# Performance work log

Hardware: AMD Instinct MI355X
Metric: run time of the kernel (lower is better)

## Reference

```python
import jax, jax.numpy as jnp
import numpy as np
import math

HIDDEN = 512
N_PROTO = 1024
BATCH = 16384


def setup_inputs() -> dict:
    key = jax.random.key(0)
    kx, kp = jax.random.split(key)
    X = jax.random.normal(kx, (BATCH, HIDDEN), dtype=jnp.float32)
    # prototypes init: uniform in [-k, k], k = 1/sqrt(hidden)
    k = 1.0 / math.sqrt(HIDDEN)
    u = jax.random.uniform(kp, (N_PROTO, HIDDEN), dtype=jnp.float32)
    prototypes = k + (-2.0 * k) * u
    return {"X": X, "prototypes": prototypes}


def reference(X, prototypes):
    # out[b, p] = -sum_h (X[b,h] - prototypes[p,h])^2
    x_sq = jnp.sum(X * X, axis=1, keepdims=True)            # [B, 1]
    p_sq = jnp.sum(prototypes * prototypes, axis=1)[None, :]  # [1, P]
    cross = jnp.einsum("bh,ph->bp", X, prototypes)          # [B, P]
    return -(x_sq + p_sq - 2.0 * cross)
```

## Files before the change

### kernel.cpp

```cpp
#include <hip/hip_runtime.h>
#include <hip/hip_bf16.h>

#define MDIM 16384
#define NDIM 1024
#define KDIM 512
#define BM 128
#define BN 128
#define BK 64
#define KTILES (KDIM / BK)

typedef __attribute__((ext_vector_type(8))) short bf16x8;
typedef __attribute__((ext_vector_type(4))) float f32x4;

__device__ __forceinline__ short f2bf(float f) {
    union { float f; unsigned u; } v; v.f = f;
    unsigned r = v.u + 0x7fff + ((v.u >> 16) & 1);
    return (short)(r >> 16);
}

__device__ __forceinline__ bf16x8 cvt8(float4 a, float4 b) {
    bf16x8 o;
    o[0] = f2bf(a.x); o[1] = f2bf(a.y); o[2] = f2bf(a.z); o[3] = f2bf(a.w);
    o[4] = f2bf(b.x); o[5] = f2bf(b.y); o[6] = f2bf(b.z); o[7] = f2bf(b.w);
    return o;
}

__device__ __forceinline__ void gload_lds16(const void* g, void* l) {
    __builtin_amdgcn_global_load_lds(
        (const __attribute__((address_space(1))) void*)g,
        (__attribute__((address_space(3))) void*)l, 16, 0, 0);
}

__global__ __launch_bounds__(256) void convert_sumsq(
        const float* __restrict__ X, const float* __restrict__ P,
        short* __restrict__ Xbf, short* __restrict__ Pbf,
        float* __restrict__ xsq, float* __restrict__ psq) {
    int wave = (blockIdx.x * blockDim.x + threadIdx.x) >> 6;
    int lane = threadIdx.x & 63;
    const float* src; short* dstb; float* dsts; int row;
    if (wave < MDIM) { src = X; dstb = Xbf; dsts = xsq; row = wave; }
    else             { src = P; dstb = Pbf; dsts = psq; row = wave - MDIM; }
    const float4* r4 = (const float4*)(src + (size_t)row * KDIM) + lane * 2;
    float4 a = r4[0], b = r4[1];
    *(bf16x8*)(dstb + (size_t)row * KDIM + lane * 8) = cvt8(a, b);
    float s = a.x*a.x + a.y*a.y + a.z*a.z + a.w*a.w
            + b.x*b.x + b.y*b.y + b.z*b.z + b.w*b.w;
    #pragma unroll
    for (int off = 32; off; off >>= 1) s += __shfl_down(s, off, 64);
    if (lane == 0) dsts[row] = s;
}

__global__ __launch_bounds__(512, 4) void dist_gemm_db(
        const short* __restrict__ Xbf, const short* __restrict__ Pbf,
        const float* __restrict__ xsq, const float* __restrict__ psq,
        float* __restrict__ out) {
    __shared__ short As[2][BM * BK];
    __shared__ short Bs[2][BN * BK];

    int tid = threadIdx.x;
    int bid = blockIdx.x;
    int swz = (bid & 7) * 128 + (bid >> 3);
    int bn = swz & 7, bm = swz >> 3;
    int row0 = bm * BM, col0 = bn * BN;

    int lane = tid & 63, wid = tid >> 6;
    int wr = wid >> 2, wc = wid & 3;

    f32x4 acc[4][2] = {};

    const short* Ab = Xbf + (size_t)row0 * KDIM;
    const short* Bb = Pbf + (size_t)col0 * KDIM;

    auto stage = [&](int sel, int kt) {
        #pragma unroll
        for (int s = 0; s < 2; ++s) {
            int c = s * 512 + tid;
            int row = c >> 3;
            int g16 = (c & 7) ^ (row & 7);
            const char* ga = (const char*)(Ab + (size_t)row * KDIM)
                             + (size_t)kt * (BK * 2) + g16 * 16;
            const char* gb = (const char*)(Bb + (size_t)row * KDIM)
                             + (size_t)kt * (BK * 2) + g16 * 16;
            char* la = (char*)&As[sel][0] + s * 8192 + wid * 1024;
            char* lb = (char*)&Bs[sel][0] + s * 8192 + wid * 1024;
            gload_lds16(ga, la);
            gload_lds16(gb, lb);
        }
    };

    auto lds_off = [&](int row, int kb) {
        return (row * (BK * 2) + kb) ^ ((row & 7) << 4);
    };

    auto compute = [&](int sel) {
        const char* aB = (const char*)&As[sel][0];
        const char* bB = (const char*)&Bs[sel][0];
        #pragma unroll
        for (int ks = 0; ks < 2; ++ks) {
            int kb = ks * 64 + ((lane >> 4) * 16);
            bf16x8 af[4], bfr[2];
            #pragma unroll
            for (int m = 0; m < 4; ++m)
                af[m] = *(const bf16x8*)(aB +
                    lds_off(wr * 64 + m * 16 + (lane & 15), kb));
            #pragma unroll
            for (int n = 0; n < 2; ++n)
                bfr[n] = *(const bf16x8*)(bB +
                    lds_off(wc * 32 + n * 16 + (lane & 15), kb));
            #pragma unroll
            for (int m = 0; m < 4; ++m)
                #pragma unroll
                for (int n = 0; n < 2; ++n)
                    acc[m][n] = __builtin_amdgcn_mfma_f32_16x16x32_bf16(
                        af[m], bfr[n], acc[m][n], 0, 0, 0);
        }
    };

    stage(0, 0);
    __syncthreads();
    int cur = 0;
    #pragma unroll
    for (int kt = 0; kt < KTILES - 1; ++kt) {
        stage(cur ^ 1, kt + 1);
        compute(cur);
        __syncthreads();
        cur ^= 1;
    }
    compute(cur);

    int cr = (lane >> 4) * 4;
    int cc = lane & 15;
    float ps[2];
    #pragma unroll
    for (int n = 0; n < 2; ++n) ps[n] = psq[col0 + wc * 32 + n * 16 + cc];
    #pragma unroll
    for (int m = 0; m < 4; ++m) {
        int grb = row0 + wr * 64 + m * 16 + cr;
        #pragma unroll
        for (int r = 0; r < 4; ++r) {
            float xv = xsq[grb + r];
            size_t ob = (size_t)(grb + r) * NDIM;
            #pragma unroll
            for (int n = 0; n < 2; ++n) {
                int gc = col0 + wc * 32 + n * 16 + cc;
                out[ob + gc] = 2.0f * acc[m][n][r] - xv - ps[n];
            }
        }
    }
}

__global__ __launch_bounds__(256) void sumsq_kernel(
        const float* __restrict__ X, const float* __restrict__ P,
        float* __restrict__ xsq, float* __restrict__ psq) {
    int wave = (blockIdx.x * blockDim.x + threadIdx.x) >> 6;
    int lane = threadIdx.x & 63;
    const float* src; float* dst; int row;
    if (wave < MDIM) { src = X; dst = xsq; row = wave; }
    else             { src = P; dst = psq; row = wave - MDIM; }
    const float4* r4 = (const float4*)(src + (size_t)row * KDIM) + lane * 2;
    float4 a = r4[0], b = r4[1];
    float s = a.x*a.x + a.y*a.y + a.z*a.z + a.w*a.w
            + b.x*b.x + b.y*b.y + b.z*b.z + b.w*b.w;
    #pragma unroll
    for (int off = 32; off; off >>= 1) s += __shfl_down(s, off, 64);
    if (lane == 0) dst[row] = s;
}

__global__ __launch_bounds__(256) void dist_gemm(
        const float* __restrict__ X, const float* __restrict__ P,
        const float* __restrict__ xsq, const float* __restrict__ psq,
        float* __restrict__ out) {
    __shared__ short As[128 * BK];
    __shared__ short Bs[128 * BK];
    int tid = threadIdx.x;
    int bid = blockIdx.x;
    int swz = (bid & 7) * 128 + (bid >> 3);
    int bn = swz & 7, bm = swz >> 3;
    int row0 = bm * 128, col0 = bn * 128;
    int lane = tid & 63, wid = tid >> 6;
    int wm = (wid >> 1) * 64, wn = (wid & 1) * 64;
    f32x4 acc[4][4] = {};
    int rbase = tid >> 3;
    int kg = tid & 7;
    const float* Abase = X + (size_t)row0 * KDIM;
    const float* Bbase = P + (size_t)col0 * KDIM;
    for (int kt = 0; kt < KDIM / BK; ++kt) {
        int kofs = kt * BK + kg * 8;
        __syncthreads();
        #pragma unroll
        for (int i = 0; i < 4; ++i) {
            int row = rbase + 32 * i;
            const float4* ga = (const float4*)(Abase + (size_t)row * KDIM + kofs);
            float4 a0 = ga[0], a1 = ga[1];
            const float4* gb = (const float4*)(Bbase + (size_t)row * KDIM + kofs);
            float4 b0 = gb[0], b1 = gb[1];
            int off = (row * (BK * 2) + kg * 16) ^ ((row & 7) << 4);
            *(bf16x8*)((char*)As + off) = cvt8(a0, a1);
            *(bf16x8*)((char*)Bs + off) = cvt8(b0, b1);
        }
        __syncthreads();
        #pragma unroll
        for (int ks = 0; ks < 2; ++ks) {
            bf16x8 af[4], bfr[4];
            int kb = ks * 64 + ((lane >> 4) * 16);
            #pragma unroll
            for (int m = 0; m < 4; ++m) {
                int row = wm + m * 16 + (lane & 15);
                int off = (row * (BK * 2) + kb) ^ ((row & 7) << 4);
                af[m] = *(const bf16x8*)((const char*)As + off);
            }
            #pragma unroll
            for (int n = 0; n < 4; ++n) {
                int row = wn + n * 16 + (lane & 15);
                int off = (row * (BK * 2) + kb) ^ ((row & 7) << 4);
                bfr[n] = *(const bf16x8*)((const char*)Bs + off);
            }
            #pragma unroll
            for (int m = 0; m < 4; ++m)
                #pragma unroll
                for (int n = 0; n < 4; ++n)
                    acc[m][n] = __builtin_amdgcn_mfma_f32_16x16x32_bf16(
                        af[m], bfr[n], acc[m][n], 0, 0, 0);
        }
    }
    int cr = (lane >> 4) * 4;
    int cc = lane & 15;
    #pragma unroll
    for (int n = 0; n < 4; ++n) {
        int gc = col0 + wn + n * 16 + cc;
        float ps = psq[gc];
        #pragma unroll
        for (int m = 0; m < 4; ++m) {
            int grb = row0 + wm + m * 16 + cr;
            #pragma unroll
            for (int r = 0; r < 4; ++r) {
                float v = 2.0f * acc[m][n][r] - xsq[grb + r] - ps;
                out[(size_t)(grb + r) * NDIM + gc] = v;
            }
        }
    }
}

extern "C" void kernel_launch(void* const* d_in, const int* in_sizes, int n_in,
                              void* d_out, int out_size, void* d_ws, size_t ws_size,
                              hipStream_t stream) {
    const float* X = (const float*)d_in[0];
    const float* P = (const float*)d_in[1];
    float* out = (float*)d_out;

    const size_t bf_elems = (size_t)(MDIM + NDIM) * KDIM;
    const size_t need = bf_elems * 2 + (size_t)(MDIM + NDIM) * 4;

    if (ws_size >= need) {
        short* Xbf = (short*)d_ws;
        short* Pbf = Xbf + (size_t)MDIM * KDIM;
        float* xsq = (float*)(Xbf + bf_elems);
        float* psq = xsq + MDIM;
        convert_sumsq<<<(MDIM + NDIM) / 4, 256, 0, stream>>>(X, P, Xbf, Pbf, xsq, psq);
        dist_gemm_db<<<(MDIM / BM) * (NDIM / BN), 512, 0, stream>>>(Xbf, Pbf, xsq, psq, out);
    } else {
        float* xsq = (float*)d_ws;
        float* psq = xsq + MDIM;
        sumsq_kernel<<<(MDIM + NDIM) / 4, 256, 0, stream>>>(X, P, xsq, psq);
        dist_gemm<<<(MDIM / 128) * (NDIM / 128), 256, 0, stream>>>(X, P, xsq, psq, out);
    }
}
```

Measured before the change: 41.10 us.

## Fuse X bf16 conversion and row norms into the distance GEMM

Removes the separate pass that converted all of X to bf16 and computed its row norms. The GEMM kernel now loads fp32 X tiles into registers, converts them and writes them into swizzled LDS, and accumulates row sums of squares on the fly. Only the prototypes still go through a small pre-conversion kernel. The block-to-tile mapping also changes so that the 8 column blocks sharing an X row block run close together. The cost is that every X tile is now read and converted 8 times (once per column block) in fp32, plus extra register pressure and VALU work inside the GEMM.

```diff
diff --git a/kernel.cpp b/kernel.cpp
--- a/kernel.cpp
+++ b/kernel.cpp
@@ -7,9 +7,10 @@
 #define BM 128
 #define BN 128
 #define BK 64
-#define KTILES (KDIM / BK)
+#define KT (KDIM / BK)
 
 typedef __attribute__((ext_vector_type(8))) short bf16x8;
+typedef __attribute__((ext_vector_type(4))) short bf16x4;
 typedef __attribute__((ext_vector_type(4))) float f32x4;
 
 __device__ __forceinline__ short f2bf(float f) {
@@ -31,67 +32,77 @@
         (__attribute__((address_space(3))) void*)l, 16, 0, 0);
 }
 
-__global__ __launch_bounds__(256) void convert_sumsq(
-        const float* __restrict__ X, const float* __restrict__ P,
-        short* __restrict__ Xbf, short* __restrict__ Pbf,
-        float* __restrict__ xsq, float* __restrict__ psq) {
+__global__ __launch_bounds__(256) void convert_p(
+        const float* __restrict__ P, short* __restrict__ Pbf,
+        float* __restrict__ psq) {
     int wave = (blockIdx.x * blockDim.x + threadIdx.x) >> 6;
     int lane = threadIdx.x & 63;
-    const float* src; short* dstb; float* dsts; int row;
-    if (wave < MDIM) { src = X; dstb = Xbf; dsts = xsq; row = wave; }
-    else             { src = P; dstb = Pbf; dsts = psq; row = wave - MDIM; }
-    const float4* r4 = (const float4*)(src + (size_t)row * KDIM) + lane * 2;
+    const float4* r4 = (const float4*)(P + (size_t)wave * KDIM) + lane * 2;
     float4 a = r4[0], b = r4[1];
-    *(bf16x8*)(dstb + (size_t)row * KDIM + lane * 8) = cvt8(a, b);
+    *(bf16x8*)(Pbf + (size_t)wave * KDIM + lane * 8) = cvt8(a, b);
     float s = a.x*a.x + a.y*a.y + a.z*a.z + a.w*a.w
             + b.x*b.x + b.y*b.y + b.z*b.z + b.w*b.w;
     #pragma unroll
     for (int off = 32; off; off >>= 1) s += __shfl_down(s, off, 64);
-    if (lane == 0) dsts[row] = s;
-}
-
-__global__ __launch_bounds__(512, 4) void dist_gemm_db(
-        const short* __restrict__ Xbf, const short* __restrict__ Pbf,
-        const float* __restrict__ xsq, const float* __restrict__ psq,
-        float* __restrict__ out) {
+    if (lane == 0) psq[wave] = s;
+}
+
+__global__ __launch_bounds__(512, 4) void dist_fused2(
+        const float* __restrict__ X, const short* __restrict__ Pbf,
+        const float* __restrict__ psq, float* __restrict__ out) {
     __shared__ short As[2][BM * BK];
     __shared__ short Bs[2][BN * BK];
+    __shared__ float xs_l[BM];
 
     int tid = threadIdx.x;
     int bid = blockIdx.x;
-    int swz = (bid & 7) * 128 + (bid >> 3);
-    int bn = swz & 7, bm = swz >> 3;
-    int row0 = bm * BM, col0 = bn * BN;
+    int x = bid & 7, j = bid >> 3;
+    int colb = j & 7, rowb = x * 16 + (j >> 3);
+    int row0 = rowb * BM, col0 = colb * BN;
 
     int lane = tid & 63, wid = tid >> 6;
     int wr = wid >> 2, wc = wid & 3;
 
     f32x4 acc[4][2] = {};
 
-    const short* Ab = Xbf + (size_t)row0 * KDIM;
+    int arow = tid >> 2, q = tid & 3;
+    const float4* rp4 = (const float4*)(X + (size_t)(row0 + arow) * KDIM);
+    float4 ra[4];
+    float ssq = 0.f;
+
+    auto loadA = [&](int kt) {
+        #pragma unroll
+        for (int i = 0; i < 4; ++i)
+            ra[i] = rp4[kt * 16 + i * 4 + q];
+    };
+    auto commitA = [&](int sel) {
+        #pragma unroll
+        for (int i = 0; i < 4; ++i) {
+            float4 a = ra[i];
+            ssq += a.x * a.x + a.y * a.y + a.z * a.z + a.w * a.w;
+            bf16x4 av;
+            av[0] = f2bf(a.x); av[1] = f2bf(a.y); av[2] = f2bf(a.z); av[3] = f2bf(a.w);
+            int col4 = i * 4 + q;
+            int off = (arow * (BK * 2) + col4 * 8) ^ ((arow & 7) << 4);
+            *(bf16x4*)((char*)&As[sel][0] + off) = av;
+        }
+    };
     const short* Bb = Pbf + (size_t)col0 * KDIM;
-
-    auto stage = [&](int sel, int kt) {
+    auto stageB = [&](int sel, int kt) {
         #pragma unroll
         for (int s = 0; s < 2; ++s) {
             int c = s * 512 + tid;
             int row = c >> 3;
             int g16 = (c & 7) ^ (row & 7);
-            const char* ga = (const char*)(Ab + (size_t)row * KDIM)
-                             + (size_t)kt * (BK * 2) + g16 * 16;
             const char* gb = (const char*)(Bb + (size_t)row * KDIM)
                              + (size_t)kt * (BK * 2) + g16 * 16;
-            char* la = (char*)&As[sel][0] + s * 8192 + wid * 1024;
-            char* lb = (char*)&Bs[sel][0] + s * 8192 + wid * 1024;
-            gload_lds16(ga, la);
-            gload_lds16(gb, lb);
+            gload_lds16(gb, (char*)&Bs[sel][0] + s * 8192 + wid * 1024);
         }
     };
 
     auto lds_off = [&](int row, int kb) {
         return (row * (BK * 2) + kb) ^ ((row & 7) << 4);
     };
-
     auto compute = [&](int sel) {
         const char* aB = (const char*)&As[sel][0];
         const char* bB = (const char*)&Bs[sel][0];
@@ -116,17 +127,26 @@
         }
     };
 
-    stage(0, 0);
+    stageB(0, 0);
+    loadA(0);
+    commitA(0);
     __syncthreads();
-    int cur = 0;
-    #pragma unroll
-    for (int kt = 0; kt < KTILES - 1; ++kt) {
-        stage(cur ^ 1, kt + 1);
+
+    #pragma unroll
+    for (int t = 0; t < KT - 1; ++t) {
+        int cur = t & 1;
+        stageB(cur ^ 1, t + 1);
+        loadA(t + 1);
         compute(cur);
+        commitA(cur ^ 1);
         __syncthreads();
-        cur ^= 1;
-    }
-    compute(cur);
+    }
+    compute((KT - 1) & 1);
+
+    ssq += __shfl_xor(ssq, 1, 64);
+    ssq += __shfl_xor(ssq, 2, 64);
+    if (q == 0) xs_l[arow] = ssq;
+    __syncthreads();
 
     int cr = (lane >> 4) * 4;
     int cc = lane & 15;
@@ -135,16 +155,14 @@
     for (int n = 0; n < 2; ++n) ps[n] = psq[col0 + wc * 32 + n * 16 + cc];
     #pragma unroll
     for (int m = 0; m < 4; ++m) {
-        int grb = row0 + wr * 64 + m * 16 + cr;
         #pragma unroll
         for (int r = 0; r < 4; ++r) {
-            float xv = xsq[grb + r];
-            size_t ob = (size_t)(grb + r) * NDIM;
-            #pragma unroll
-            for (int n = 0; n < 2; ++n) {
-                int gc = col0 + wc * 32 + n * 16 + cc;
-                out[ob + gc] = 2.0f * acc[m][n][r] - xv - ps[n];
-            }
+            int lr = wr * 64 + m * 16 + cr + r;
+            float xv = xs_l[lr];
+            size_t ob = (size_t)(row0 + lr) * NDIM + col0;
+            #pragma unroll
+            for (int n = 0; n < 2; ++n)
+                out[ob + wc * 32 + n * 16 + cc] = 2.0f * acc[m][n][r] - xv - ps[n];
         }
     }
 }
@@ -248,16 +266,13 @@
     const float* P = (const float*)d_in[1];
     float* out = (float*)d_out;
 
-    const size_t bf_elems = (size_t)(MDIM + NDIM) * KDIM;
-    const size_t need = bf_elems * 2 + (size_t)(MDIM + NDIM) * 4;
+    const size_t need = (size_t)NDIM * KDIM * 2 + (size_t)NDIM * 4;
 
     if (ws_size >= need) {
-        short* Xbf = (short*)d_ws;
-        short* Pbf = Xbf + (size_t)MDIM * KDIM;
-        float* xsq = (float*)(Xbf + bf_elems);
-        float* psq = xsq + MDIM;
-        convert_sumsq<<<(MDIM + NDIM) / 4, 256, 0, stream>>>(X, P, Xbf, Pbf, xsq, psq);
-        dist_gemm_db<<<(MDIM / BM) * (NDIM / BN), 512, 0, stream>>>(Xbf, Pbf, xsq, psq, out);
+        short* Pbf = (short*)d_ws;
+        float* psq = (float*)(Pbf + (size_t)NDIM * KDIM);
+        convert_p<<<NDIM / 4, 256, 0, stream>>>(P, Pbf, psq);
+        dist_fused2<<<(MDIM / BM) * (NDIM / BN), 512, 0, stream>>>(X, Pbf, psq, out);
     } else {
         float* xsq = (float*)d_ws;
         float* psq = xsq + MDIM;
```

After: 104.9 us. 155% more time.
